# Kernel tuning notes

Measured on AMD Instinct MI355X. Metric: run time of the kernel, lower is better.

Reference implementation:

```python
import jax, jax.numpy as jnp
import numpy as np
from jax import lax

B, T, I, H, L = 64, 256, 512, 1024, 2


def setup_inputs() -> dict:
    key = jax.random.key(0)
    ks = jax.random.split(key, 6)
    s = 0.05  # small init scale for numerical stability
    return {
        "x": jax.random.normal(ks[0], (B, T, I), dtype=jnp.float32),
        "h0": jnp.zeros((L, B, H), dtype=jnp.float32),
        "c0": jnp.zeros((L, B, H), dtype=jnp.float32),
        "W_ih_0": jax.random.normal(ks[1], (I, 4 * H), dtype=jnp.float32) * s,
        "W_hh_0": jax.random.normal(ks[2], (H, 4 * H), dtype=jnp.float32) * s,
        "b_0": jnp.zeros((4 * H,), dtype=jnp.float32),
        "W_ih_1": jax.random.normal(ks[3], (H, 4 * H), dtype=jnp.float32) * s,
        "W_hh_1": jax.random.normal(ks[4], (H, 4 * H), dtype=jnp.float32) * s,
        "b_1": jnp.zeros((4 * H,), dtype=jnp.float32),
    }


def _lstm_layer(x_tbd, h0, c0, W_ih, W_hh, b):
    """x_tbd: [T, B, in]; returns ([T, B, H], h_T, c_T). Standard (Zaremba) LSTM cell."""
    def step(carry, xt):
        h, c = carry
        gates = xt @ W_ih + h @ W_hh + b  # [B, 4H]
        i, f, g, o = jnp.split(gates, 4, axis=-1)
        i = jax.nn.sigmoid(i)
        f = jax.nn.sigmoid(f)
        g = jnp.tanh(g)
        o = jax.nn.sigmoid(o)
        c_new = f * c + i * g
        h_new = o * jnp.tanh(c_new)
        return (h_new, c_new), h_new

    (h_T, c_T), ys = lax.scan(step, (h0, c0), x_tbd)
    return ys, h_T, c_T


def reference(x, h0, c0, W_ih_0, W_hh_0, b_0, W_ih_1, W_hh_1, b_1):
    # x: [B, T, I] batch-first as in the torch module; scan over time.
    xt = jnp.swapaxes(x, 0, 1)  # [T, B, I]
    weights = [(W_ih_0, W_hh_0, b_0), (W_ih_1, W_hh_1, b_1)]
    hs, cs = [], []
    values = xt
    for l in range(L):
        W_ih, W_hh, b = weights[l]
        values, h_T, c_T = _lstm_layer(values, h0[l], c0[l], W_ih, W_hh, b)
        hs.append(h_T)
        cs.append(c_T)
    outputs = jnp.swapaxes(values, 0, 1)  # [B, T, H]
    return outputs, jnp.stack(hs, 0), jnp.stack(cs, 0)
```

## Files before the change

### kernel.cpp

```cpp
#include <hip/hip_runtime.h>
#include <hip/hip_bf16.h>

typedef __attribute__((ext_vector_type(8))) short short8;
typedef __attribute__((ext_vector_type(4))) float f32x4;

constexpr int BB = 64;
constexpr int TT = 256;
constexpr int II = 512;
constexpr int HH = 1024;

constexpr int NBLK = 256;
constexpr int NTHR = 512;

constexpr int HTILE = (HH / 8) * BB * 8;
constexpr int XTILE = (II / 8) * BB * 8;

constexpr size_t OFF_FLAGS = 0;
constexpr size_t OFF_WIH0T = 4096;
constexpr size_t OFF_WHH0T = OFF_WIH0T + (size_t)4096 * 512 * 2;
constexpr size_t OFF_WIH1T = OFF_WHH0T + (size_t)4096 * 1024 * 2;
constexpr size_t OFF_WHH1T = OFF_WIH1T + (size_t)4096 * 1024 * 2;
constexpr size_t OFF_XT    = OFF_WHH1T + (size_t)4096 * 1024 * 2;
constexpr size_t OFF_H0D   = OFF_XT + (size_t)TT * XTILE * 2;
constexpr size_t OFF_H1D   = OFF_H0D + (size_t)4 * HTILE * 2;

__device__ __forceinline__ float sigmoid_(float x) {
  return 1.f / (1.f + __expf(-x));
}
__device__ __forceinline__ float tanh_(float x) {
  float ax = fabsf(x);
  float e = __expf(-2.f * ax);
  float t = (1.f - e) / (1.f + e);
  return copysignf(t, x);
}

__global__ void zero_flags(int* f) { f[threadIdx.x] = 0; }

__global__ void transpose_to_bf16(const float* __restrict__ src,
                                  __hip_bfloat16* __restrict__ dst,
                                  int K, int N) {
  __shared__ float tile[64][65];
  const int n0 = blockIdx.x * 64;
  const int k0 = blockIdx.y * 64;
  const int tx = threadIdx.x & 63;
  const int ty = threadIdx.x >> 6;
#pragma unroll
  for (int i = 0; i < 64; i += 4)
    tile[ty + i][tx] = src[(size_t)(k0 + ty + i) * N + n0 + tx];
  __syncthreads();
#pragma unroll
  for (int i = 0; i < 64; i += 4) {
    const int n = ty + i;
    dst[(size_t)(n0 + n) * K + k0 + tx] = __float2bfloat16(tile[tx][n]);
  }
}

__global__ void tile_x(const float* __restrict__ x, __hip_bfloat16* __restrict__ xt) {
  const int t = blockIdx.x;
  const int k = threadIdx.x;
  __hip_bfloat16* o = xt + (size_t)t * XTILE;
  for (int b = 0; b < BB; ++b) {
    float v = x[((size_t)b * TT + t) * II + k];
    o[(k >> 3) * (BB * 8) + b * 8 + (k & 7)] = __float2bfloat16(v);
  }
}

__global__ void init_h(const float* __restrict__ h0, __hip_bfloat16* h0d, __hip_bfloat16* h1d) {
  const int idx = blockIdx.x * 256 + threadIdx.x;
  const int l = idx >> 16;
  const int b = (idx >> 10) & 63;
  const int j = idx & 1023;
  __hip_bfloat16 v = __float2bfloat16(h0[idx]);
  __hip_bfloat16* dst = l ? h1d : h0d;
  dst[(j >> 3) * (BB * 8) + b * 8 + (j & 7)] = v;
}

template <int KI, int KW, int LAYER>
__device__ __forceinline__ void scan_impl(
    const __hip_bfloat16* __restrict__ xsrc,
    const __hip_bfloat16* __restrict__ WiT,
    const __hip_bfloat16* __restrict__ WhT,
    const float* __restrict__ bias,
    const float* __restrict__ c0_in,
    __hip_bfloat16* h0d, __hip_bfloat16* h1d,
    float* __restrict__ out, int* flags, float (*part)[2][4][64][4],
    int bhalf, int jbase) {
  const int tid = threadIdx.x;
  const int wave = tid >> 6;
  const int lane = tid & 63;
  const int cc = lane & 15;
  const int lrow = lane >> 4;

  const int kbase = wave * (KW * 32);

  short8 Bf[KW][4];
#pragma unroll
  for (int w = 0; w < KW; ++w) {
    const int kg = kbase + w * 32 + lrow * 8;
#pragma unroll
    for (int g = 0; g < 4; ++g) {
      const int gcol = g * HH + jbase + cc;
      const __hip_bfloat16* p;
      if (kg < KI) p = WiT + (size_t)gcol * KI + kg;
      else         p = WhT + (size_t)gcol * HH + (kg - KI);
      Bf[w][g] = *(const short8*)p;
    }
  }

  int nfl, throff;
  int* fbase;
  if constexpr (LAYER == 0) {
    const int lo = kbase, hi = kbase + KW * 32;
    const int hlo = lo > KI ? lo : KI;
    const int hhi = hi > KI ? hi : KI;
    nfl = (hhi - hlo) >> 4;
    fbase = flags + bhalf * 64 + ((hlo - KI) >> 4);
    throff = 0;
  } else {
    if (kbase < KI) {
      nfl = 16;
      fbase = flags + bhalf * 64 + (kbase >> 4);
      throff = 1;
    } else {
      nfl = 16;
      fbase = flags + 128 + bhalf * 64 + ((kbase - KI) >> 4);
      throff = 0;
    }
  }
  const int fidx = (lane < nfl) ? lane : (nfl > 0 ? nfl - 1 : 0);
  int l1min = 0;

  const int ejl = tid & 15;
  const int ebl = tid >> 4;
  const int ej = jbase + ejl;
  const int eb = bhalf * 32 + ebl;
  const int pm = ebl >> 4, psub = (ebl >> 2) & 3, pr = ebl & 3;
  const int plane = psub * 16 + ejl;
  const float bi = bias[ej];
  const float bf_ = bias[HH + ej];
  const float bg = bias[2 * HH + ej];
  const float bo = bias[3 * HH + ej];
  float cst = c0_in[(size_t)LAYER * BB * HH + (size_t)eb * HH + ej];

  for (int p = 0; p < TT; ++p) {
    if constexpr (LAYER == 0) {
      if (wave < 2) {
        const int thr = p - 3;
        if (thr > l1min) {
          int* fp = flags + 128 + bhalf * 64 + lane;
          for (;;) {
            int v = __hip_atomic_load(fp, __ATOMIC_RELAXED, __HIP_MEMORY_SCOPE_AGENT);
            int m = v;
            m = min(m, __shfl_xor(m, 32));
            m = min(m, __shfl_xor(m, 16));
            m = min(m, __shfl_xor(m, 8));
            m = min(m, __shfl_xor(m, 4));
            m = min(m, __shfl_xor(m, 2));
            m = min(m, __shfl_xor(m, 1));
            if (m >= thr) { l1min = m; break; }
            __builtin_amdgcn_s_sleep(2);
          }
        }
      }
    }
    if (nfl > 0) {
      const int thr = p + throff;
      int* fp = fbase + fidx;
      for (;;) {
        int v = __hip_atomic_load(fp, __ATOMIC_RELAXED, __HIP_MEMORY_SCOPE_AGENT);
        if (__all(v >= thr)) break;
        __builtin_amdgcn_s_sleep(2);
      }
    }
    __syncthreads();
    if (wave == 0)
      __builtin_amdgcn_fence(__ATOMIC_ACQUIRE, "agent");
    __syncthreads();

    const __hip_bfloat16* px;
    const __hip_bfloat16* ph;
    __hip_bfloat16* hout;
    if constexpr (LAYER == 0) {
      px = xsrc + (size_t)p * XTILE;
      ph = h0d + (size_t)(p & 3) * HTILE;
      hout = h0d + (size_t)((p + 1) & 3) * HTILE;
    } else {
      px = h0d + (size_t)((p + 1) & 3) * HTILE;
      ph = h1d + (size_t)(p & 3) * HTILE;
      hout = h1d + (size_t)((p + 1) & 3) * HTILE;
    }

    f32x4 acc[2][4] = {};
    short8 abuf[4][2];

    auto issue_pair = [&](int w, short8* dst) {
      const int kg = kbase + w * 32;
      const __hip_bfloat16* ab;
      int kc;
      if (kg < KI) { ab = px; kc = (kg >> 3) + lrow; }
      else         { ab = ph; kc = ((kg - KI) >> 3) + lrow; }
#pragma unroll
      for (int m = 0; m < 2; ++m) {
        const __hip_bfloat16* ptr =
            ab + (size_t)kc * (BB * 8) + (size_t)(bhalf * 32 + m * 16 + cc) * 8;
        asm volatile("global_load_dwordx4 %0, %1, off" : "=v"(dst[m]) : "v"(ptr));
      }
    };

#pragma unroll
    for (int w = 0; w < 4; ++w) issue_pair(w, abuf[w]);

#pragma unroll
    for (int w = 0; w < KW; ++w) {
      const int op = (KW - w < 4) ? (KW - w) : 4;
      const int vm = 2 * (op - 1);
      if (vm == 6)      asm volatile("s_waitcnt vmcnt(6)" ::: "memory");
      else if (vm == 4) asm volatile("s_waitcnt vmcnt(4)" ::: "memory");
      else if (vm == 2) asm volatile("s_waitcnt vmcnt(2)" ::: "memory");
      else              asm volatile("s_waitcnt vmcnt(0)" ::: "memory");
      __builtin_amdgcn_sched_barrier(0);
#pragma unroll
      for (int m = 0; m < 2; ++m)
#pragma unroll
        for (int g = 0; g < 4; ++g)
          acc[m][g] = __builtin_amdgcn_mfma_f32_16x16x32_bf16(
              abuf[w & 3][m], Bf[w][g], acc[m][g], 0, 0, 0);
      if (w + 4 < KW) issue_pair(w + 4, abuf[w & 3]);
    }

#pragma unroll
    for (int m = 0; m < 2; ++m)
#pragma unroll
      for (int g = 0; g < 4; ++g)
        *(f32x4*)&part[wave][m][g][lane][0] = acc[m][g];
    __syncthreads();

    {
      float s0 = 0.f, s1 = 0.f, s2 = 0.f, s3 = 0.f;
#pragma unroll
      for (int w = 0; w < 8; ++w) {
        s0 += part[w][pm][0][plane][pr];
        s1 += part[w][pm][1][plane][pr];
        s2 += part[w][pm][2][plane][pr];
        s3 += part[w][pm][3][plane][pr];
      }
      float iv = sigmoid_(s0 + bi);
      float fv = sigmoid_(s1 + bf_);
      float gv = tanh_(s2 + bg);
      float ov = sigmoid_(s3 + bo);
      float cn = fv * cst + iv * gv;
      cst = cn;
      float hv = ov * tanh_(cn);
      __hip_bfloat16 hb = __float2bfloat16(hv);
      unsigned short hu = *reinterpret_cast<unsigned short*>(&hb);
      unsigned pu = (unsigned)__shfl_xor((int)hu, 1);
      if ((tid & 1) == 0) {
        uint32_t packed = (uint32_t)hu | ((pu & 0xffffu) << 16);
        uint32_t* hq = (uint32_t*)hout;
        __hip_atomic_store(hq + (ej >> 3) * 256 + eb * 4 + ((ej & 7) >> 1), packed,
                           __ATOMIC_RELAXED, __HIP_MEMORY_SCOPE_AGENT);
      }
      if constexpr (LAYER == 1)
        out[((size_t)eb * TT + p) * HH + ej] = hv;
      if (p == TT - 1) {
        out[(size_t)BB * TT * HH + (size_t)LAYER * BB * HH + (size_t)eb * HH + ej] = hv;
        out[(size_t)BB * TT * HH + (size_t)2 * BB * HH + (size_t)LAYER * BB * HH + (size_t)eb * HH + ej] = cn;
      }
    }
    asm volatile("s_waitcnt vmcnt(0)" ::: "memory");
    __syncthreads();
    if (tid == 0)
      __hip_atomic_store(&flags[blockIdx.x], p + 1, __ATOMIC_RELAXED, __HIP_MEMORY_SCOPE_AGENT);
  }
}

__global__ __launch_bounds__(NTHR, 2) void lstm_scan(
    const __hip_bfloat16* __restrict__ xt,
    const __hip_bfloat16* __restrict__ Wih0T, const __hip_bfloat16* __restrict__ Whh0T,
    const __hip_bfloat16* __restrict__ Wih1T, const __hip_bfloat16* __restrict__ Whh1T,
    const float* __restrict__ b0, const float* __restrict__ b1,
    const float* __restrict__ c0_in,
    __hip_bfloat16* h0d, __hip_bfloat16* h1d,
    float* __restrict__ out, int* flags) {
  __shared__ float part[8][2][4][64][4];
  const int blk = blockIdx.x;
  const int jslot = blk & 63;
  const int bhalf = (blk >> 6) & 1;
  const int jbase = jslot * 16;
  if ((blk >> 7) == 0)
    scan_impl<512, 6, 0>(xt, Wih0T, Whh0T, b0, c0_in, h0d, h1d, out, flags, part, bhalf, jbase);
  else
    scan_impl<1024, 8, 1>(nullptr, Wih1T, Whh1T, b1, c0_in, h0d, h1d, out, flags, part, bhalf, jbase);
}

extern "C" void kernel_launch(void* const* d_in, const int* in_sizes, int n_in,
                              void* d_out, int out_size, void* d_ws, size_t ws_size,
                              hipStream_t stream) {
  (void)in_sizes; (void)n_in; (void)out_size; (void)ws_size;
  const float* x    = (const float*)d_in[0];
  const float* h0   = (const float*)d_in[1];
  const float* c0   = (const float*)d_in[2];
  const float* Wih0 = (const float*)d_in[3];
  const float* Whh0 = (const float*)d_in[4];
  const float* b0   = (const float*)d_in[5];
  const float* Wih1 = (const float*)d_in[6];
  const float* Whh1 = (const float*)d_in[7];
  const float* b1   = (const float*)d_in[8];
  float* out = (float*)d_out;
  char* ws = (char*)d_ws;

  int* flags = (int*)(ws + OFF_FLAGS);
  __hip_bfloat16* wih0t = (__hip_bfloat16*)(ws + OFF_WIH0T);
  __hip_bfloat16* whh0t = (__hip_bfloat16*)(ws + OFF_WHH0T);
  __hip_bfloat16* wih1t = (__hip_bfloat16*)(ws + OFF_WIH1T);
  __hip_bfloat16* whh1t = (__hip_bfloat16*)(ws + OFF_WHH1T);
  __hip_bfloat16* xt    = (__hip_bfloat16*)(ws + OFF_XT);
  __hip_bfloat16* h0d   = (__hip_bfloat16*)(ws + OFF_H0D);
  __hip_bfloat16* h1d   = (__hip_bfloat16*)(ws + OFF_H1D);

  zero_flags<<<1, 256, 0, stream>>>(flags);
  transpose_to_bf16<<<dim3(64, 8),  256, 0, stream>>>(Wih0, wih0t, 512, 4096);
  transpose_to_bf16<<<dim3(64, 16), 256, 0, stream>>>(Whh0, whh0t, 1024, 4096);
  transpose_to_bf16<<<dim3(64, 16), 256, 0, stream>>>(Wih1, wih1t, 1024, 4096);
  transpose_to_bf16<<<dim3(64, 16), 256, 0, stream>>>(Whh1, whh1t, 1024, 4096);
  tile_x<<<TT, 512, 0, stream>>>(x, xt);
  init_h<<<512, 256, 0, stream>>>(h0, h0d, h1d);
  lstm_scan<<<NBLK, NTHR, 0, stream>>>(xt, wih0t, whh0t, wih1t, whh1t,
                                       b0, b1, c0, h0d, h1d, out, flags);
}
```

Before: 1.826 ms.

## Replace fine-grained per-slice flag waits with global wavefront barrier and XCD-leader cache invalidation

Changes the per-block dependency polling on specific flag ranges into a global barrier over all 256 block flags per wavefront step. Layer 1 now runs one step behind layer 0 in the same wavefront index tau. Acquire fences are restricted to one leader block per XCD, elected through an atomic counter. Other blocks rely on buffer_inv sc0 and sc0 loads on the h paths. The LDS partial-sum layout is also transposed and padded to cut bank conflicts, and the flag store moves before the output writes. In exchange, the global barrier removes the pipelining slack between layers, and correctness depends on the leader-fence and cache-invalidate scheme.

```diff
diff --git a/kernel.cpp b/kernel.cpp
--- a/kernel.cpp
+++ b/kernel.cpp
@@ -34,7 +34,7 @@
   return copysignf(t, x);
 }
 
-__global__ void zero_flags(int* f) { f[threadIdx.x] = 0; }
+__global__ void zero_flags(int* f) { f[blockIdx.x * 256 + threadIdx.x] = 0; }
 
 __global__ void transpose_to_bf16(const float* __restrict__ src,
                                   __hip_bfloat16* __restrict__ dst,
@@ -83,8 +83,8 @@
     const float* __restrict__ bias,
     const float* __restrict__ c0_in,
     __hip_bfloat16* h0d, __hip_bfloat16* h1d,
-    float* __restrict__ out, int* flags, float (*part)[2][4][64][4],
-    int bhalf, int jbase) {
+    float* __restrict__ out, int* flags, float (*part)[2][4][4][65],
+    int bhalf, int jbase, bool leader) {
   const int tid = threadIdx.x;
   const int wave = tid >> 6;
   const int lane = tid & 63;
@@ -106,29 +106,6 @@
       Bf[w][g] = *(const short8*)p;
     }
   }
-
-  int nfl, throff;
-  int* fbase;
-  if constexpr (LAYER == 0) {
-    const int lo = kbase, hi = kbase + KW * 32;
-    const int hlo = lo > KI ? lo : KI;
-    const int hhi = hi > KI ? hi : KI;
-    nfl = (hhi - hlo) >> 4;
-    fbase = flags + bhalf * 64 + ((hlo - KI) >> 4);
-    throff = 0;
-  } else {
-    if (kbase < KI) {
-      nfl = 16;
-      fbase = flags + bhalf * 64 + (kbase >> 4);
-      throff = 1;
-    } else {
-      nfl = 16;
-      fbase = flags + 128 + bhalf * 64 + ((kbase - KI) >> 4);
-      throff = 0;
-    }
-  }
-  const int fidx = (lane < nfl) ? lane : (nfl > 0 ? nfl - 1 : 0);
-  int l1min = 0;
 
   const int ejl = tid & 15;
   const int ebl = tid >> 4;
@@ -142,107 +119,99 @@
   const float bo = bias[3 * HH + ej];
   float cst = c0_in[(size_t)LAYER * BB * HH + (size_t)eb * HH + ej];
 
-  for (int p = 0; p < TT; ++p) {
-    if constexpr (LAYER == 0) {
-      if (wave < 2) {
-        const int thr = p - 3;
-        if (thr > l1min) {
-          int* fp = flags + 128 + bhalf * 64 + lane;
-          for (;;) {
-            int v = __hip_atomic_load(fp, __ATOMIC_RELAXED, __HIP_MEMORY_SCOPE_AGENT);
-            int m = v;
-            m = min(m, __shfl_xor(m, 32));
-            m = min(m, __shfl_xor(m, 16));
-            m = min(m, __shfl_xor(m, 8));
-            m = min(m, __shfl_xor(m, 4));
-            m = min(m, __shfl_xor(m, 2));
-            m = min(m, __shfl_xor(m, 1));
-            if (m >= thr) { l1min = m; break; }
-            __builtin_amdgcn_s_sleep(2);
-          }
-        }
-      }
-    }
-    if (nfl > 0) {
-      const int thr = p + throff;
-      int* fp = fbase + fidx;
+  for (int tau = 0; tau <= TT; ++tau) {
+    if (tau > 0 && wave == 0) {
       for (;;) {
-        int v = __hip_atomic_load(fp, __ATOMIC_RELAXED, __HIP_MEMORY_SCOPE_AGENT);
-        if (__all(v >= thr)) break;
+        int v0 = __hip_atomic_load(&flags[lane],       __ATOMIC_RELAXED, __HIP_MEMORY_SCOPE_AGENT);
+        int v1 = __hip_atomic_load(&flags[lane + 64],  __ATOMIC_RELAXED, __HIP_MEMORY_SCOPE_AGENT);
+        int v2 = __hip_atomic_load(&flags[lane + 128], __ATOMIC_RELAXED, __HIP_MEMORY_SCOPE_AGENT);
+        int v3 = __hip_atomic_load(&flags[lane + 192], __ATOMIC_RELAXED, __HIP_MEMORY_SCOPE_AGENT);
+        int mn = min(min(v0, v1), min(v2, v3));
+        if (__all(mn >= tau)) break;
         __builtin_amdgcn_s_sleep(2);
       }
     }
     __syncthreads();
-    if (wave == 0)
+    asm volatile("s_waitcnt vmcnt(0)" ::: "memory");
+    if (leader && wave == 0)
       __builtin_amdgcn_fence(__ATOMIC_ACQUIRE, "agent");
-    __syncthreads();
-
-    const __hip_bfloat16* px;
-    const __hip_bfloat16* ph;
-    __hip_bfloat16* hout;
-    if constexpr (LAYER == 0) {
-      px = xsrc + (size_t)p * XTILE;
-      ph = h0d + (size_t)(p & 3) * HTILE;
-      hout = h0d + (size_t)((p + 1) & 3) * HTILE;
-    } else {
-      px = h0d + (size_t)((p + 1) & 3) * HTILE;
-      ph = h1d + (size_t)(p & 3) * HTILE;
-      hout = h1d + (size_t)((p + 1) & 3) * HTILE;
-    }
-
-    f32x4 acc[2][4] = {};
-    short8 abuf[4][2];
-
-    auto issue_pair = [&](int w, short8* dst) {
-      const int kg = kbase + w * 32;
-      const __hip_bfloat16* ab;
-      int kc;
-      if (kg < KI) { ab = px; kc = (kg >> 3) + lrow; }
-      else         { ab = ph; kc = ((kg - KI) >> 3) + lrow; }
-#pragma unroll
-      for (int m = 0; m < 2; ++m) {
-        const __hip_bfloat16* ptr =
-            ab + (size_t)kc * (BB * 8) + (size_t)(bhalf * 32 + m * 16 + cc) * 8;
-        asm volatile("global_load_dwordx4 %0, %1, off" : "=v"(dst[m]) : "v"(ptr));
-      }
-    };
-
-#pragma unroll
-    for (int w = 0; w < 4; ++w) issue_pair(w, abuf[w]);
-
-#pragma unroll
-    for (int w = 0; w < KW; ++w) {
-      const int op = (KW - w < 4) ? (KW - w) : 4;
-      const int vm = 2 * (op - 1);
-      if (vm == 6)      asm volatile("s_waitcnt vmcnt(6)" ::: "memory");
-      else if (vm == 4) asm volatile("s_waitcnt vmcnt(4)" ::: "memory");
-      else if (vm == 2) asm volatile("s_waitcnt vmcnt(2)" ::: "memory");
-      else              asm volatile("s_waitcnt vmcnt(0)" ::: "memory");
-      __builtin_amdgcn_sched_barrier(0);
+    asm volatile("buffer_inv sc0" ::: "memory");
+    __builtin_amdgcn_sched_barrier(0);
+
+    const bool active = (LAYER == 0) ? (tau < TT) : (tau >= 1);
+    if (active) {
+      const int p = (LAYER == 0) ? tau : tau - 1;
+      const __hip_bfloat16* px;
+      const __hip_bfloat16* ph;
+      __hip_bfloat16* hout;
+      if constexpr (LAYER == 0) {
+        px = xsrc + (size_t)p * XTILE;
+        ph = h0d + (size_t)(p & 3) * HTILE;
+        hout = h0d + (size_t)((p + 1) & 3) * HTILE;
+      } else {
+        px = h0d + (size_t)((p + 1) & 3) * HTILE;
+        ph = h1d + (size_t)(p & 3) * HTILE;
+        hout = h1d + (size_t)((p + 1) & 3) * HTILE;
+      }
+
+      f32x4 acc[2][4] = {};
+      short8 abuf[4][2];
+
+      auto issue_pair = [&](int w, short8* dst) {
+        const int kg = kbase + w * 32;
+        const __hip_bfloat16* ab;
+        int kc;
+        bool hpath;
+        if (kg < KI) { ab = px; kc = (kg >> 3) + lrow; hpath = (LAYER == 1); }
+        else         { ab = ph; kc = ((kg - KI) >> 3) + lrow; hpath = true; }
+#pragma unroll
+        for (int m = 0; m < 2; ++m) {
+          const __hip_bfloat16* ptr =
+              ab + (size_t)kc * (BB * 8) + (size_t)(bhalf * 32 + m * 16 + cc) * 8;
+          if (hpath)
+            asm volatile("global_load_dwordx4 %0, %1, off sc0" : "=v"(dst[m]) : "v"(ptr));
+          else
+            asm volatile("global_load_dwordx4 %0, %1, off" : "=v"(dst[m]) : "v"(ptr));
+        }
+      };
+
+#pragma unroll
+      for (int w = 0; w < 4; ++w) issue_pair(w, abuf[w]);
+
+#pragma unroll
+      for (int w = 0; w < KW; ++w) {
+        const int op = (KW - w < 4) ? (KW - w) : 4;
+        const int vm = 2 * (op - 1);
+        if (vm == 6)      asm volatile("s_waitcnt vmcnt(6)" ::: "memory");
+        else if (vm == 4) asm volatile("s_waitcnt vmcnt(4)" ::: "memory");
+        else if (vm == 2) asm volatile("s_waitcnt vmcnt(2)" ::: "memory");
+        else              asm volatile("s_waitcnt vmcnt(0)" ::: "memory");
+        __builtin_amdgcn_sched_barrier(0);
+#pragma unroll
+        for (int m = 0; m < 2; ++m)
+#pragma unroll
+          for (int g = 0; g < 4; ++g)
+            acc[m][g] = __builtin_amdgcn_mfma_f32_16x16x32_bf16(
+                abuf[w & 3][m], Bf[w][g], acc[m][g], 0, 0, 0);
+        if (w + 4 < KW) issue_pair(w + 4, abuf[w & 3]);
+      }
+
 #pragma unroll
       for (int m = 0; m < 2; ++m)
 #pragma unroll
         for (int g = 0; g < 4; ++g)
-          acc[m][g] = __builtin_amdgcn_mfma_f32_16x16x32_bf16(
-              abuf[w & 3][m], Bf[w][g], acc[m][g], 0, 0, 0);
-      if (w + 4 < KW) issue_pair(w + 4, abuf[w & 3]);
-    }
-
-#pragma unroll
-    for (int m = 0; m < 2; ++m)
-#pragma unroll
-      for (int g = 0; g < 4; ++g)
-        *(f32x4*)&part[wave][m][g][lane][0] = acc[m][g];
-    __syncthreads();
-
-    {
+#pragma unroll
+          for (int r = 0; r < 4; ++r)
+            part[wave][m][g][r][lane] = acc[m][g][r];
+      __syncthreads();
+
       float s0 = 0.f, s1 = 0.f, s2 = 0.f, s3 = 0.f;
 #pragma unroll
       for (int w = 0; w < 8; ++w) {
-        s0 += part[w][pm][0][plane][pr];
-        s1 += part[w][pm][1][plane][pr];
-        s2 += part[w][pm][2][plane][pr];
-        s3 += part[w][pm][3][plane][pr];
+        s0 += part[w][pm][0][pr][plane];
+        s1 += part[w][pm][1][pr][plane];
+        s2 += part[w][pm][2][pr][plane];
+        s3 += part[w][pm][3][pr][plane];
       }
       float iv = sigmoid_(s0 + bi);
       float fv = sigmoid_(s1 + bf_);
@@ -260,17 +229,21 @@
         __hip_atomic_store(hq + (ej >> 3) * 256 + eb * 4 + ((ej & 7) >> 1), packed,
                            __ATOMIC_RELAXED, __HIP_MEMORY_SCOPE_AGENT);
       }
+      asm volatile("s_waitcnt vmcnt(0)" ::: "memory");
+      __syncthreads();
+      if (tid == 0)
+        __hip_atomic_store(&flags[blockIdx.x], tau + 1, __ATOMIC_RELAXED, __HIP_MEMORY_SCOPE_AGENT);
       if constexpr (LAYER == 1)
         out[((size_t)eb * TT + p) * HH + ej] = hv;
       if (p == TT - 1) {
         out[(size_t)BB * TT * HH + (size_t)LAYER * BB * HH + (size_t)eb * HH + ej] = hv;
         out[(size_t)BB * TT * HH + (size_t)2 * BB * HH + (size_t)LAYER * BB * HH + (size_t)eb * HH + ej] = cn;
       }
+    } else {
+      __syncthreads();
+      if (tid == 0)
+        __hip_atomic_store(&flags[blockIdx.x], tau + 1, __ATOMIC_RELAXED, __HIP_MEMORY_SCOPE_AGENT);
     }
-    asm volatile("s_waitcnt vmcnt(0)" ::: "memory");
-    __syncthreads();
-    if (tid == 0)
-      __hip_atomic_store(&flags[blockIdx.x], p + 1, __ATOMIC_RELAXED, __HIP_MEMORY_SCOPE_AGENT);
   }
 }
 
@@ -282,15 +255,26 @@
     const float* __restrict__ c0_in,
     __hip_bfloat16* h0d, __hip_bfloat16* h1d,
     float* __restrict__ out, int* flags) {
-  __shared__ float part[8][2][4][64][4];
+  __shared__ float part[8][2][4][4][65];
+  __shared__ int s_leader;
+  if (threadIdx.x == 0) {
+    unsigned xcd;
+    asm volatile("s_getreg_b32 %0, hwreg(HW_REG_XCC_ID)" : "=s"(xcd));
+    int t = __hip_atomic_fetch_add(&flags[256 + (xcd & 15)], 1,
+                                   __ATOMIC_RELAXED, __HIP_MEMORY_SCOPE_AGENT);
+    s_leader = (t == 0);
+  }
+  __syncthreads();
+  const bool leader = (s_leader != 0);
+
   const int blk = blockIdx.x;
   const int jslot = blk & 63;
   const int bhalf = (blk >> 6) & 1;
   const int jbase = jslot * 16;
   if ((blk >> 7) == 0)
-    scan_impl<512, 6, 0>(xt, Wih0T, Whh0T, b0, c0_in, h0d, h1d, out, flags, part, bhalf, jbase);
+    scan_impl<512, 6, 0>(xt, Wih0T, Whh0T, b0, c0_in, h0d, h1d, out, flags, part, bhalf, jbase, leader);
   else
-    scan_impl<1024, 8, 1>(nullptr, Wih1T, Whh1T, b1, c0_in, h0d, h1d, out, flags, part, bhalf, jbase);
+    scan_impl<1024, 8, 1>(nullptr, Wih1T, Whh1T, b1, c0_in, h0d, h1d, out, flags, part, bhalf, jbase, leader);
 }
 
 extern "C" void kernel_launch(void* const* d_in, const int* in_sizes, int n_in,
@@ -314,17 +298,17 @@
   __hip_bfloat16* whh0t = (__hip_bfloat16*)(ws + OFF_WHH0T);
   __hip_bfloat16* wih1t = (__hip_bfloat16*)(ws + OFF_WIH1T);
   __hip_bfloat16* whh1t = (__hip_bfloat16*)(ws + OFF_WHH1T);
-  __hip_bfloat16* xt    = (__hip_bfloat16*)(ws + OFF_XT);
+  __hip_bfloat16* xtl   = (__hip_bfloat16*)(ws + OFF_XT);
   __hip_bfloat16* h0d   = (__hip_bfloat16*)(ws + OFF_H0D);
   __hip_bfloat16* h1d   = (__hip_bfloat16*)(ws + OFF_H1D);
 
-  zero_flags<<<1, 256, 0, stream>>>(flags);
+  zero_flags<<<2, 256, 0, stream>>>(flags);
   transpose_to_bf16<<<dim3(64, 8),  256, 0, stream>>>(Wih0, wih0t, 512, 4096);
   transpose_to_bf16<<<dim3(64, 16), 256, 0, stream>>>(Whh0, whh0t, 1024, 4096);
   transpose_to_bf16<<<dim3(64, 16), 256, 0, stream>>>(Wih1, wih1t, 1024, 4096);
   transpose_to_bf16<<<dim3(64, 16), 256, 0, stream>>>(Whh1, whh1t, 1024, 4096);
-  tile_x<<<TT, 512, 0, stream>>>(x, xt);
+  tile_x<<<TT, 512, 0, stream>>>(x, xtl);
   init_h<<<512, 256, 0, stream>>>(h0, h0d, h1d);
-  lstm_scan<<<NBLK, NTHR, 0, stream>>>(xt, wih0t, whh0t, wih1t, whh1t,
+  lstm_scan<<<NBLK, NTHR, 0, stream>>>(xtl, wih0t, whh0t, wih1t, whh1t,
                                        b0, b1, c0, h0d, h1d, out, flags);
 }
```

After: 1.682 ms. 7.8% less time.
